# Kernel tuning notes

Hardware: AMD Instinct MI355X
Metric: run time of the kernel (lower is better)

Reference implementation:

```python
import math
import jax, jax.numpy as jnp
import numpy as np
from jax import lax

B, T, D, S, N_SLOTS, N_ITERS = 16, 4096, 768, 768, 16, 8
THR, EPS = 0.5, 1e-8
SCALE = D ** -0.5
NEG = -jnp.finfo(jnp.float32).max


def ln(x, g, b):
    mu = x.mean(-1, keepdims=True)
    var = ((x - mu) ** 2).mean(-1, keepdims=True)
    return (x - mu) / jnp.sqrt(var + 1e-5) * g + b


def gru_cell(u, h, wih, whh, bih, bhh):
    # torch GRUCell: r,z,n gate ordering
    gi = u @ wih.T + bih
    gh = h @ whh.T + bhh
    ir, iz, inn = jnp.split(gi, 3, axis=-1)
    hr, hz, hn = jnp.split(gh, 3, axis=-1)
    r = jax.nn.sigmoid(ir + hr)
    z = jax.nn.sigmoid(iz + hz)
    n = jnp.tanh(inn + r * hn)
    return (1.0 - z) * n + z * h


def sa_step(slots, k, v, p, slot_mask, context_mask):
    q = ln(slots, p['lsg'], p['lsb']) @ p['Wq'].T
    dots = jnp.einsum('bid,bjd->bij', q, k) * SCALE  # [B, n_slots, T]
    dots = jnp.where(context_mask[:, None, :], dots, NEG)
    if slot_mask is not None:
        dots = jnp.where(slot_mask[:, :, None], dots, NEG)
    attn_vis = jax.nn.softmax(dots, axis=1)  # softmax over SLOTS (inverted attn)
    attn = attn_vis + EPS
    attn = attn / attn.sum(-1, keepdims=True)
    updates = jnp.einsum('bjd,bij->bid', v, attn)
    b, n, d = slots.shape
    h = gru_cell(updates.reshape(b * n, d), slots.reshape(b * n, d),
                 p['gwih'], p['gwhh'], p['gbih'], p['gbhh'])
    slots = h.reshape(b, n, d)
    pre = ln(slots, p['lfg'], p['lfb'])
    slots = slots + (jax.nn.relu(pre @ p['w1'].T + p['b1']) @ p['w2'].T + p['b2'])
    return slots, attn_vis


def cluster_single(slots, attn, slot_mask):
    sl = lax.stop_gradient(slots)  # torch no_grad block
    ns = sl / jnp.clip(jnp.linalg.norm(sl, axis=-1, keepdims=True), 1e-12)
    smm = (slot_mask[:, :, None] & slot_mask[:, None, :]).astype(jnp.float32)
    dist = 1.0 - jnp.einsum('bnd,bmd->bnm', ns, ns)
    dist = jnp.where(smm > 0, dist, 2.0)
    adj = (dist < THR).astype(jnp.float32) * smm
    for _ in range(math.ceil(math.log2(N_SLOTS))):  # transitive closure by squaring
        adj = jnp.minimum(adj @ adj, 1.0) * smm
    cum = jnp.cumsum(adj, axis=1)
    cm = adj * (cum <= 1.0)  # keep first row of each connected component
    counts = (cm > 0).any(axis=2).sum(axis=1)
    reset = counts < 3
    eye = jnp.eye(N_SLOTS, dtype=jnp.float32)[None] * slot_mask[:, :, None].astype(jnp.float32)
    cm = jnp.where(reset[:, None, None], eye, cm)
    cw = cm / jnp.clip(cm.sum(axis=2, keepdims=True), 1.0)
    cm = lax.stop_gradient(cm)
    cw = lax.stop_gradient(cw)
    means = cw @ slots          # grads flow through slots only
    cattn = cm @ attn           # grads flow through attn only
    out_mask = (cm > 0).any(axis=2) & slot_mask
    return means, cattn, out_mask


def setup_inputs() -> dict:
    key = jax.random.key(0)
    ks = jax.random.split(key, 16)
    sc = 0.02
    return {
        'x': jax.random.normal(ks[0], (B, T, D), jnp.float32),
        'context_mask': jnp.ones((B, T), jnp.bool_),
        'n_slots': N_SLOTS,
        'slots_init': jax.random.normal(ks[1], (N_SLOTS, S), jnp.float32),
        'Wk': jax.random.normal(ks[2], (S, D), jnp.float32) * sc,
        'Wv': jax.random.normal(ks[3], (S, D), jnp.float32) * sc,
        'Wq': jax.random.normal(ks[4], (S, S), jnp.float32) * sc,
        'gwih': jax.random.normal(ks[5], (3 * S, S), jnp.float32) * sc,
        'gwhh': jax.random.normal(ks[6], (3 * S, S), jnp.float32) * sc,
        'gbih': jnp.zeros((3 * S,), jnp.float32),
        'gbhh': jnp.zeros((3 * S,), jnp.float32),
        'w1': jax.random.normal(ks[7], (4 * S, S), jnp.float32) * sc,
        'b1': jnp.zeros((4 * S,), jnp.float32),
        'w2': jax.random.normal(ks[8], (S, 4 * S), jnp.float32) * sc,
        'b2': jnp.zeros((S,), jnp.float32),
        'lin_g': jnp.ones((D,), jnp.float32), 'lin_b': jnp.zeros((D,), jnp.float32),
        'lsg': jnp.ones((S,), jnp.float32), 'lsb': jnp.zeros((S,), jnp.float32),
        'lfg': jnp.ones((S,), jnp.float32), 'lfb': jnp.zeros((S,), jnp.float32),
    }


def reference(x, context_mask, n_slots, slots_init, Wk, Wv, Wq, gwih, gwhh,
              gbih, gbhh, w1, b1, w2, b2, lin_g, lin_b, lsg, lsb, lfg, lfb):
    p = dict(Wq=Wq, gwih=gwih, gwhh=gwhh, gbih=gbih, gbhh=gbhh,
             w1=w1, b1=b1, w2=w2, b2=b2, lsg=lsg, lsb=lsb, lfg=lfg, lfb=lfb)
    xn = ln(x, lin_g, lin_b)
    init_slots = jnp.broadcast_to(slots_init[None], (x.shape[0], N_SLOTS, S))
    k = xn @ Wk.T
    v = xn @ Wv.T
    slots = init_slots
    for _ in range(N_ITERS):
        slots, attn = sa_step(slots, k, v, p, None, context_mask)
    # implicit differentiation trick
    slots = lax.stop_gradient(slots) - lax.stop_gradient(init_slots) + init_slots
    slot_mask = jnp.ones((x.shape[0], N_SLOTS), jnp.bool_)
    slots, attn = sa_step(slots, k, v, p, slot_mask, context_mask)
    slots, attn, slot_mask = cluster_single(slots, attn, slot_mask)
    attn_map = jnp.transpose(attn, (0, 2, 1))  # [B, T, n_slots]
    return slots, attn_map, slot_mask
```

## Files before the change

kernel.cpp:

```cpp
#include <hip/hip_runtime.h>
#include <hip/hip_bf16.h>

typedef __hip_bfloat16 bf16;
typedef __attribute__((ext_vector_type(4))) float f32x4;
typedef __attribute__((ext_vector_type(8))) short s16x8;
typedef unsigned int u32;
typedef unsigned short u16;

#define B_ 16
#define T_ 4096
#define D_ 768
#define S_ 768
#define NS 16
#define NIT 9
#define NCHUNK 16
#define TCH 256
#define EPS 1e-8f
#define SCALE 0.036084391824351615f

__device__ __forceinline__ void gld16(const void* g, void* l) {
    __builtin_amdgcn_global_load_lds((const __attribute__((address_space(1))) u32*)g,
                                     (__attribute__((address_space(3))) u32*)l, 16, 0, 0);
}

__device__ __forceinline__ u16 bfbits(float x) {
    bf16 h = __float2bfloat16(x);
    return *reinterpret_cast<u16*>(&h);
}

__global__ void __launch_bounds__(256) cvt_all_kernel(
    const float* __restrict__ wq, const float* __restrict__ wk, const float* __restrict__ wv,
    const float* __restrict__ gwih, const float* __restrict__ gwhh,
    const float* __restrict__ w1, const float* __restrict__ w2,
    bf16* __restrict__ wq_b, bf16* __restrict__ wkv_b,
    bf16* __restrict__ gwih_b, bf16* __restrict__ gwhh_b,
    bf16* __restrict__ w1_b, bf16* __restrict__ w2_b)
{
    int i = blockIdx.x * 256 + threadIdx.x;
    const int NW = 589824, NG = 1769472, NM = 2359296;
    if (i < NW) { wq_b[i] = __float2bfloat16(wq[i]); return; }
    i -= NW;
    if (i < NW) { wkv_b[i] = __float2bfloat16(wk[i]); return; }
    i -= NW;
    if (i < NW) { wkv_b[NW + i] = __float2bfloat16(wv[i]); return; }
    i -= NW;
    if (i < NG) { gwih_b[i] = __float2bfloat16(gwih[i]); return; }
    i -= NG;
    if (i < NG) { gwhh_b[i] = __float2bfloat16(gwhh[i]); return; }
    i -= NG;
    if (i < NM) { w1_b[i] = __float2bfloat16(w1[i]); return; }
    i -= NM;
    w2_b[i] = __float2bfloat16(w2[i]);
}

__global__ void __launch_bounds__(256) ln768_kernel(
    const float* __restrict__ x, const float* __restrict__ g,
    const float* __restrict__ bta, bf16* __restrict__ out)
{
    int row = blockIdx.x;
    int tid = threadIdx.x;
    const float* xr = x + (size_t)row * 768;
    float v0 = xr[tid], v1 = xr[tid + 256], v2 = xr[tid + 512];
    float s = v0 + v1 + v2;
    int lane = tid & 63, wid = tid >> 6;
    #pragma unroll
    for (int off = 32; off; off >>= 1) s += __shfl_down(s, off);
    __shared__ float red[4];
    __shared__ float sh_mu, sh_rs;
    if (lane == 0) red[wid] = s;
    __syncthreads();
    if (tid == 0) sh_mu = (red[0] + red[1] + red[2] + red[3]) * (1.f / 768.f);
    __syncthreads();
    float mu = sh_mu;
    float d0 = v0 - mu, d1 = v1 - mu, d2 = v2 - mu;
    float q = d0 * d0 + d1 * d1 + d2 * d2;
    #pragma unroll
    for (int off = 32; off; off >>= 1) q += __shfl_down(q, off);
    if (lane == 0) red[wid] = q;
    __syncthreads();
    if (tid == 0) sh_rs = rsqrtf((red[0] + red[1] + red[2] + red[3]) * (1.f / 768.f) + 1e-5f);
    __syncthreads();
    float rs = sh_rs;
    bf16* orow = out + (size_t)row * 768;
    orow[tid]       = __float2bfloat16(d0 * rs * g[tid]       + bta[tid]);
    orow[tid + 256] = __float2bfloat16(d1 * rs * g[tid + 256] + bta[tid + 256]);
    orow[tid + 512] = __float2bfloat16(d2 * rs * g[tid + 512] + bta[tid + 512]);
}

__global__ void __launch_bounds__(512) gemm256_kernel(
    const bf16* __restrict__ A, const bf16* __restrict__ W,
    bf16* __restrict__ kout, bf16* __restrict__ vTout, float* __restrict__ vsum)
{
    __shared__ char smem[49152];
    __shared__ float vs_l[128];
    bf16* As = (bf16*)smem;
    bf16* Bs = (bf16*)(smem + 32768);
    int tid = threadIdx.x, lane = tid & 63, wid = tid >> 6;
    int bid = blockIdx.x;
    int xcd = bid & 7, idx = bid >> 3;
    int mt = xcd * 32 + idx / 12;
    int nt = idx % 12;
    int bm0 = mt * 256, bn0 = nt * 128;
    int wr = wid >> 1, wc = wid & 1;
    int g = lane >> 4, r15 = lane & 15;
    const f32x4 vzero = {0.f, 0.f, 0.f, 0.f};
    f32x4 acc[4][4];
    #pragma unroll
    for (int m = 0; m < 4; ++m)
        #pragma unroll
        for (int n = 0; n < 4; ++n) acc[m][n] = vzero;

    for (int kt = 0; kt < 768; kt += 64) {
        __syncthreads();
        #pragma unroll
        for (int i = 0; i < 4; ++i) {
            int s0 = i * 512 + wid * 64;
            int o = (s0 + lane) * 16;
            int r = o >> 7, cb = o & 127;
            int cbs = cb ^ ((r & 7) << 4);
            gld16(A + (size_t)(bm0 + r) * 768 + kt + (cbs >> 1), (char*)As + (size_t)s0 * 16);
        }
        #pragma unroll
        for (int i = 0; i < 2; ++i) {
            int s0 = i * 512 + wid * 64;
            int o = (s0 + lane) * 16;
            int r = o >> 7, cb = o & 127;
            int cbs = cb ^ ((r & 7) << 4);
            gld16(W + (size_t)(bn0 + r) * 768 + kt + (cbs >> 1), (char*)Bs + (size_t)s0 * 16);
        }
        asm volatile("s_waitcnt vmcnt(0)" ::: "memory");
        __syncthreads();
        #pragma unroll
        for (int kk2 = 0; kk2 < 2; ++kk2) {
            s16x8 af[4], bfr[4];
            #pragma unroll
            for (int m = 0; m < 4; ++m) {
                int r = wr * 64 + m * 16 + r15;
                int p = r * 128 + ((kk2 * 64 + g * 16) ^ ((r & 7) << 4));
                af[m] = *(const s16x8*)((const char*)As + p);
            }
            #pragma unroll
            for (int n = 0; n < 4; ++n) {
                int r = wc * 64 + n * 16 + r15;
                int p = r * 128 + ((kk2 * 64 + g * 16) ^ ((r & 7) << 4));
                bfr[n] = *(const s16x8*)((const char*)Bs + p);
            }
            #pragma unroll
            for (int m = 0; m < 4; ++m)
                #pragma unroll
                for (int n = 0; n < 4; ++n)
                    acc[m][n] = __builtin_amdgcn_mfma_f32_16x16x32_bf16(af[m], bfr[n], acc[m][n], 0, 0, 0);
        }
    }

    bool is_v = (bn0 >= 768);
    float* Ct = (float*)smem;
    int bq = bm0 >> 12;
    int tloc = bm0 & 4095;
    if (is_v && tid < 128) vs_l[tid] = 0.f;
    #pragma unroll
    for (int q = 0; q < 4; ++q) {
        __syncthreads();
        if (wr == q) {
            #pragma unroll
            for (int m = 0; m < 4; ++m)
                #pragma unroll
                for (int n = 0; n < 4; ++n)
                    #pragma unroll
                    for (int j = 0; j < 4; ++j)
                        Ct[(m * 16 + g * 4 + j) * 132 + wc * 64 + n * 16 + r15] = acc[m][n][j];
        }
        __syncthreads();
        if (!is_v) {
            int r = tid >> 3, cq = tid & 7;
            u16 tmp[16];
            #pragma unroll
            for (int i = 0; i < 16; ++i) tmp[i] = bfbits(Ct[r * 132 + cq * 16 + i]);
            s16x8 o0, o1;
            #pragma unroll
            for (int i = 0; i < 8; ++i) { o0[i] = (short)tmp[i]; o1[i] = (short)tmp[8 + i]; }
            bf16* dst = kout + (size_t)(bm0 + q * 64 + r) * 768 + bn0 + cq * 16;
            *(s16x8*)dst = o0;
            *(s16x8*)(dst + 8) = o1;
        } else {
            int d = tid >> 2, tq = tid & 3;
            float ssum = 0.f;
            u16 tmp[16];
            #pragma unroll
            for (int i = 0; i < 16; ++i) {
                float f = Ct[(tq * 16 + i) * 132 + d];
                ssum += f;
                tmp[i] = bfbits(f);
            }
            s16x8 o0, o1;
            #pragma unroll
            for (int i = 0; i < 8; ++i) { o0[i] = (short)tmp[i]; o1[i] = (short)tmp[8 + i]; }
            bf16* dst = vTout + ((size_t)bq * 768 + (bn0 - 768) + d) * (size_t)T_
                        + tloc + q * 64 + tq * 16;
            *(s16x8*)dst = o0;
            *(s16x8*)(dst + 8) = o1;
            atomicAdd(&vs_l[d], ssum);
        }
    }
    if (is_v) {
        __syncthreads();
        if (tid < 128) atomicAdd(vsum + bq * 768 + (bn0 - 768) + tid, vs_l[tid]);
    }
}

__global__ void init_slots_kernel(const float* __restrict__ si,
                                  float* __restrict__ slots, bf16* __restrict__ slots_bf)
{
    int idx = blockIdx.x * 256 + threadIdx.x;
    float v = si[idx % (NS * S_)];
    slots[idx] = v;
    slots_bf[idx] = __float2bfloat16(v);
}

__global__ void __launch_bounds__(256) ln_gemm_kernel(
    const float* __restrict__ xin, const float* __restrict__ gam, const float* __restrict__ bet,
    const bf16* __restrict__ W, const float* __restrict__ bias,
    bf16* __restrict__ out, int N, int relu)
{
    __shared__ bf16 As[16 * 768];
    __shared__ bf16 Ws[2][64 * 64];
    int tid = threadIdx.x;
    int bx = blockIdx.x, bn0 = blockIdx.y * 64;
    int row = tid >> 4, li = tid & 15;
    const float* xr = xin + (size_t)(bx * 16 + row) * 768;
    float vals[48];
    float s = 0.f;
    #pragma unroll
    for (int i = 0; i < 48; ++i) { vals[i] = xr[li + i * 16]; s += vals[i]; }
    #pragma unroll
    for (int m = 1; m < 16; m <<= 1) s += __shfl_xor(s, m);
    float mu = s * (1.f / 768.f);
    float q = 0.f;
    #pragma unroll
    for (int i = 0; i < 48; ++i) { float d = vals[i] - mu; q += d * d; }
    #pragma unroll
    for (int m = 1; m < 16; m <<= 1) q += __shfl_xor(q, m);
    float rs = rsqrtf(q * (1.f / 768.f) + 1e-5f);
    #pragma unroll
    for (int i = 0; i < 48; ++i) {
        int c = li + i * 16;
        float v = (vals[i] - mu) * rs * gam[c] + bet[c];
        *(u16*)((char*)As + row * 1536 + ((c * 2) ^ ((row & 7) << 4))) = bfbits(v);
    }
    int lane = tid & 63, wid = tid >> 6;
    int g = lane >> 4, s15 = lane & 15;
    auto stageW = [&](int kt, int buf) {
        #pragma unroll
        for (int i = 0; i < 2; ++i) {
            int s0 = i * 256 + wid * 64;
            int o = (s0 + lane) * 16;
            int r = o >> 7, cb = o & 127;
            int cbs = cb ^ ((r & 7) << 4);
            gld16(W + (size_t)(bn0 + r) * 768 + kt + (cbs >> 1),
                  (char*)Ws[buf] + (size_t)s0 * 16);
        }
    };
    stageW(0, 0);
    asm volatile("s_waitcnt vmcnt(0)" ::: "memory");
    __syncthreads();
    f32x4 acc = {0.f, 0.f, 0.f, 0.f};
    int rb = wid * 16 + s15;
    for (int t = 0; t < 12; ++t) {
        int cur = t & 1;
        if (t < 11) stageW((t + 1) * 64, cur ^ 1);
        #pragma unroll
        for (int kk2 = 0; kk2 < 2; ++kk2) {
            int kabs = t * 64 + kk2 * 32;
            s16x8 af = *(const s16x8*)((const char*)As + s15 * 1536 +
                                       ((kabs * 2 + g * 16) ^ ((s15 & 7) << 4)));
            s16x8 bf_ = *(const s16x8*)((const char*)Ws[cur] + rb * 128 +
                                        ((kk2 * 64 + g * 16) ^ ((rb & 7) << 4)));
            acc = __builtin_amdgcn_mfma_f32_16x16x32_bf16(af, bf_, acc, 0, 0, 0);
        }
        asm volatile("s_waitcnt vmcnt(0)" ::: "memory");
        __syncthreads();
    }
    int cn = bn0 + rb;
    float bv = bias ? bias[cn] : 0.f;
    #pragma unroll
    for (int j = 0; j < 4; ++j) {
        float val = acc[j] + bv;
        if (relu) val = fmaxf(val, 0.f);
        out[(size_t)(bx * 16 + g * 4 + j) * N + cn] = __float2bfloat16(val);
    }
}

__device__ __forceinline__ void skinny_body(
    const bf16* A, const bf16* Bm, const float* bias, const float* Cin,
    float* Cf, bf16* Cb, int N, int K, int bm0, int bn0, int relu,
    bf16* As, bf16* Bs)
{
    int tid = threadIdx.x, lane = tid & 63, wid = tid >> 6;
    int g = lane >> 4, r15 = lane & 15;
    f32x4 acc = {0.f, 0.f, 0.f, 0.f};
    for (int kt = 0; kt < K; kt += 64) {
        __syncthreads();
        #pragma unroll
        for (int i = 0; i < 3; ++i) {
            int s0 = i * 256 + wid * 64;
            if (s0 < 640) {
                int o = (s0 + lane) * 16;
                if (o < 2048) {
                    int r = o >> 7, cb = o & 127;
                    int cbs = cb ^ ((r & 7) << 4);
                    gld16(A + (size_t)(bm0 + r) * K + kt + (cbs >> 1), (char*)As + (size_t)s0 * 16);
                } else {
                    int ob = o - 2048;
                    int r = ob >> 7, cb = ob & 127;
                    int cbs = cb ^ ((r & 7) << 4);
                    gld16(Bm + (size_t)(bn0 + r) * K + kt + (cbs >> 1),
                          (char*)Bs + (size_t)(s0 * 16 - 2048));
                }
            }
        }
        asm volatile("s_waitcnt vmcnt(0)" ::: "memory");
        __syncthreads();
        #pragma unroll
        for (int kk = 0; kk < 64; kk += 32) {
            int pa = r15 * 128 + ((kk * 2 + g * 16) ^ ((r15 & 7) << 4));
            s16x8 af = *(const s16x8*)((const char*)As + pa);
            int rb = wid * 16 + r15;
            int pb = rb * 128 + ((kk * 2 + g * 16) ^ ((rb & 7) << 4));
            s16x8 bfr = *(const s16x8*)((const char*)Bs + pb);
            acc = __builtin_amdgcn_mfma_f32_16x16x32_bf16(af, bfr, acc, 0, 0, 0);
        }
    }
    int cn = bn0 + wid * 16 + r15;
    float bv = bias ? bias[cn] : 0.f;
    #pragma unroll
    for (int j = 0; j < 4; ++j) {
        int cm = bm0 + g * 4 + j;
        size_t ci = (size_t)cm * N + cn;
        float val = acc[j] + bv;
        if (Cin) val += Cin[ci];
        if (relu) val = fmaxf(val, 0.f);
        if (Cf) Cf[ci] = val;
        if (Cb) Cb[ci] = __float2bfloat16(val);
    }
}

__global__ void __launch_bounds__(256) mlp2_kernel(
    const bf16* __restrict__ h1, const bf16* __restrict__ W2, const float* __restrict__ b2,
    const float* __restrict__ slotsB, float* __restrict__ slotsA, bf16* __restrict__ slotsA_bf)
{
    __shared__ bf16 As[16 * 64];
    __shared__ bf16 Bs[64 * 64];
    skinny_body(h1, W2, b2, slotsB, slotsA, slotsA_bf, 768, 3072,
                blockIdx.x * 16, blockIdx.y * 64, 0, As, Bs);
}

__global__ void __launch_bounds__(256) gru_gemm_kernel(
    const bf16* __restrict__ upd, const bf16* __restrict__ slots_bf,
    const bf16* __restrict__ Wih, const bf16* __restrict__ Whh,
    const float* __restrict__ bih, const float* __restrict__ bhh,
    float* __restrict__ gi, float* __restrict__ gh)
{
    __shared__ bf16 As[16 * 64];
    __shared__ bf16 Bs[64 * 64];
    int y = blockIdx.y;
    if (y < 36)
        skinny_body(upd, Wih, bih, nullptr, gi, nullptr, 2304, 768,
                    blockIdx.x * 16, y * 64, 0, As, Bs);
    else
        skinny_body(slots_bf, Whh, bhh, nullptr, gh, nullptr, 2304, 768,
                    blockIdx.x * 16, (y - 36) * 64, 0, As, Bs);
}

__global__ void __launch_bounds__(256) fused_attn_kernel(
    const bf16* __restrict__ q_bf, const bf16* __restrict__ k_bf, const bf16* __restrict__ vT,
    float* __restrict__ pU, float* __restrict__ prs, float* __restrict__ avis, int write_avis)
{
    __shared__ char smem[131072];
    bf16* ks0 = (bf16*)smem;
    bf16* ks1 = (bf16*)(smem + 49152);
    bf16* qs  = (bf16*)(smem + 98304);
    char* aL  = smem + 122880;
    __shared__ float rsw[2][16];
    int tid = threadIdx.x, lane = tid & 63, wid = tid >> 6;
    int b = blockIdx.x >> 4, chunk = blockIdx.x & 15;
    int t0 = chunk * TCH;
    int g = lane >> 4, s15 = lane & 15;
    const bf16* qb  = q_bf + (size_t)b * 16 * 768;
    const bf16* kb  = k_bf + (size_t)b * T_ * 768;
    const bf16* vtb = vT + (size_t)b * 768 * T_;

    auto stage_k = [&](int tb, bf16* dst) {
        #pragma unroll
        for (int i = 0; i < 12; ++i) {
            int s0 = i * 256 + wid * 64;
            int o = (s0 + lane) * 16;
            int r = o / 1536, cb = o % 1536;
            int cbs = cb ^ ((r & 7) << 4);
            gld16(kb + (size_t)(tb + r) * 768 + (cbs >> 1), (char*)dst + (size_t)s0 * 16);
        }
    };
    auto stage_v = [&](int tb, bf16* dst) {
        #pragma unroll
        for (int i = 0; i < 12; ++i) {
            int s0 = i * 256 + wid * 64;
            int o = (s0 + lane) * 16;
            int d = o >> 6, cb = o & 63;
            int cbs = cb ^ ((d & 3) << 4);
            gld16(vtb + (size_t)d * T_ + tb + (cbs >> 1), (char*)dst + (size_t)s0 * 16);
        }
    };

    #pragma unroll
    for (int i = 0; i < 6; ++i) {
        int s0 = i * 256 + wid * 64;
        int o = (s0 + lane) * 16;
        int r = o / 1536, cb = o % 1536;
        int cbs = cb ^ ((r & 7) << 4);
        gld16(qb + (size_t)r * 768 + (cbs >> 1), (char*)qs + (size_t)s0 * 16);
    }
    stage_k(t0, ks0);
    asm volatile("s_waitcnt vmcnt(0)" ::: "memory");
    __syncthreads();

    const f32x4 vzero = {0.f, 0.f, 0.f, 0.f};
    float rs_acc = 0.f;

    for (int ts = 0; ts < 8; ++ts) {
        bf16* cur = (ts & 1) ? ks1 : ks0;
        bf16* nxt = (ts & 1) ? ks0 : ks1;
        if (ts < 7) stage_k(t0 + (ts + 1) * 32, nxt);
        if (wid < 2) {
            f32x4 dacc = vzero;
            #pragma unroll
            for (int kk = 0; kk < 768; kk += 32) {
                int rk = wid * 16 + s15;
                int pk = rk * 1536 + ((kk * 2 + g * 16) ^ ((rk & 7) << 4));
                s16x8 kf = *(const s16x8*)((const char*)cur + pk);
                int pq = s15 * 1536 + ((kk * 2 + g * 16) ^ ((s15 & 7) << 4));
                s16x8 qf = *(const s16x8*)((const char*)qs + pq);
                dacc = __builtin_amdgcn_mfma_f32_16x16x32_bf16(kf, qf, dacc, 0, 0, 0);
            }
            float d0 = dacc[0] * SCALE, d1 = dacc[1] * SCALE,
                  d2 = dacc[2] * SCALE, d3 = dacc[3] * SCALE;
            float m0 = d0, m1 = d1, m2 = d2, m3 = d3;
            #pragma unroll
            for (int off = 1; off < 16; off <<= 1) {
                m0 = fmaxf(m0, __shfl_xor(m0, off));
                m1 = fmaxf(m1, __shfl_xor(m1, off));
                m2 = fmaxf(m2, __shfl_xor(m2, off));
                m3 = fmaxf(m3, __shfl_xor(m3, off));
            }
            float e0 = expf(d0 - m0), e1 = expf(d1 - m1), e2 = expf(d2 - m2), e3 = expf(d3 - m3);
            float q0 = e0, q1 = e1, q2 = e2, q3 = e3;
            #pragma unroll
            for (int off = 1; off < 16; off <<= 1) {
                q0 += __shfl_xor(q0, off);
                q1 += __shfl_xor(q1, off);
                q2 += __shfl_xor(q2, off);
                q3 += __shfl_xor(q3, off);
            }
            float a0 = e0 / q0, a1 = e1 / q1, a2 = e2 / q2, a3 = e3 / q3;
            rs_acc += a0 + a1 + a2 + a3;
            int tl = wid * 16 + g * 4;
            ushort2 p0, p1;
            p0.x = bfbits(a0); p0.y = bfbits(a1);
            p1.x = bfbits(a2); p1.y = bfbits(a3);
            int sw = (s15 & 3) << 4;
            char* aS = aL + ts * 1024;
            *(ushort2*)(aS + s15 * 64 + ((tl * 2) ^ sw))       = p0;
            *(ushort2*)(aS + s15 * 64 + (((tl + 2) * 2) ^ sw)) = p1;
            if (write_avis) {
                f32x4 w = {a0, a1, a2, a3};
                *(f32x4*)(avis + (size_t)(b * 16 + s15) * T_ + t0 + ts * 32 + tl) = w;
            }
        }
        asm volatile("s_waitcnt vmcnt(0)" ::: "memory");
        __syncthreads();
    }

    f32x4 uacc[12];
    #pragma unroll
    for (int i = 0; i < 12; ++i) uacc[i] = vzero;
    stage_v(t0, ks0);
    asm volatile("s_waitcnt vmcnt(0)" ::: "memory");
    __syncthreads();
    for (int ts = 0; ts < 8; ++ts) {
        bf16* cur = (ts & 1) ? ks1 : ks0;
        bf16* nxt = (ts & 1) ? ks0 : ks1;
        if (ts < 7) stage_v(t0 + (ts + 1) * 32, nxt);
        {
            int pa = ts * 1024 + s15 * 64 + ((g * 16) ^ ((s15 & 3) << 4));
            s16x8 afr = *(const s16x8*)(aL + pa);
            #pragma unroll
            for (int i = 0; i < 12; ++i) {
                int d = (wid * 12 + i) * 16 + s15;
                int pv = d * 64 + ((g * 16) ^ ((d & 3) << 4));
                s16x8 vf = *(const s16x8*)((const char*)cur + pv);
                uacc[i] = __builtin_amdgcn_mfma_f32_16x16x32_bf16(vf, afr, uacc[i], 0, 0, 0);
            }
        }
        asm volatile("s_waitcnt vmcnt(0)" ::: "memory");
        __syncthreads();
    }

    float* pUb = pU + (size_t)(b * 16 + chunk) * 768 * 16;
    #pragma unroll
    for (int i = 0; i < 12; ++i) {
        int dbase = (wid * 12 + i) * 16 + g * 4;
        #pragma unroll
        for (int j = 0; j < 4; ++j)
            pUb[(size_t)(dbase + j) * 16 + s15] = uacc[i][j];
    }
    rs_acc += __shfl_xor(rs_acc, 16);
    rs_acc += __shfl_xor(rs_acc, 32);
    if (wid < 2 && lane < 16) rsw[wid][s15] = rs_acc;
    __syncthreads();
    if (tid < 16) prs[(b * 16 + chunk) * 16 + tid] = rsw[0][tid] + rsw[1][tid];
}

__global__ void __launch_bounds__(256) attn_reduce_kernel(
    const float* __restrict__ pU, const float* __restrict__ prs,
    const float* __restrict__ vsum, bf16* __restrict__ upd)
{
    int idx = blockIdx.x * 256 + threadIdx.x;
    int d = idx % 768;
    int s = (idx / 768) & 15;
    int b = idx / (768 * 16);
    float su = 0.f;
    #pragma unroll
    for (int c = 0; c < 16; ++c) su += pU[((size_t)(b * 16 + c) * 768 + d) * 16 + s];
    float rs = 0.f;
    #pragma unroll
    for (int c = 0; c < 16; ++c) rs += prs[(b * 16 + c) * 16 + s];
    float val = (su + EPS * vsum[b * 768 + d]) / (rs + T_ * EPS);
    upd[idx] = __float2bfloat16(val);
}

__global__ void __launch_bounds__(256) gru_gates_kernel(
    const float* __restrict__ gi, const float* __restrict__ gh,
    const float* __restrict__ slotsA, float* __restrict__ slotsB)
{
    int idx = blockIdx.x * 256 + threadIdx.x;
    int r = idx / 768, c = idx - r * 768;
    const float* gir = gi + (size_t)r * 2304;
    const float* ghr = gh + (size_t)r * 2304;
    float ir = gir[c], iz = gir[768 + c], inn = gir[1536 + c];
    float hr = ghr[c], hz = ghr[768 + c], hn  = ghr[1536 + c];
    float rg = 1.f / (1.f + expf(-(ir + hr)));
    float z  = 1.f / (1.f + expf(-(iz + hz)));
    float n  = tanhf(inn + rg * hn);
    float h  = slotsA[idx];
    slotsB[idx] = (1.f - z) * n + z * h;
}

__global__ void __launch_bounds__(256) cluster_kernel(
    const float* __restrict__ slots, float* __restrict__ out_slots,
    float* __restrict__ out_mask, float* __restrict__ cm_g)
{
    int b = blockIdx.x;
    __shared__ float s[16][768];
    __shared__ float inv[16];
    __shared__ float adj[16][16], tmp[16][16], cw[16][16];
    __shared__ int reset_s;
    const float* sb = slots + (size_t)b * 16 * 768;
    for (int i = threadIdx.x; i < 16 * 768; i += 256) s[i / 768][i % 768] = sb[i];
    __syncthreads();
    if (threadIdx.x < 16) {
        float q = 0.f;
        for (int d = 0; d < 768; ++d) q += s[threadIdx.x][d] * s[threadIdx.x][d];
        inv[threadIdx.x] = 1.f / fmaxf(sqrtf(q), 1e-12f);
    }
    __syncthreads();
    int n = threadIdx.x >> 4, m = threadIdx.x & 15;
    float dot = 0.f;
    for (int d = 0; d < 768; ++d) dot += s[n][d] * s[m][d];
    dot *= inv[n] * inv[m];
    adj[n][m] = ((1.f - dot) < 0.5f) ? 1.f : 0.f;
    __syncthreads();
    #pragma unroll
    for (int it = 0; it < 4; ++it) {
        float t = 0.f;
        #pragma unroll
        for (int j = 0; j < 16; ++j) t += adj[n][j] * adj[j][m];
        tmp[n][m] = fminf(t, 1.f);
        __syncthreads();
        adj[n][m] = tmp[n][m];
        __syncthreads();
    }
    if (threadIdx.x < 16) {
        int mm = threadIdx.x;
        float run = 0.f;
        for (int nn = 0; nn < 16; ++nn) {
            run += adj[nn][mm];
            tmp[nn][mm] = adj[nn][mm] * ((run <= 1.f) ? 1.f : 0.f);
        }
    }
    __syncthreads();
    if (threadIdx.x == 0) {
        int cnt = 0;
        for (int nn = 0; nn < 16; ++nn) {
            bool any = false;
            for (int j = 0; j < 16; ++j) any = any || (tmp[nn][j] > 0.f);
            cnt += any ? 1 : 0;
        }
        reset_s = (cnt < 3) ? 1 : 0;
    }
    __syncthreads();
    if (reset_s) tmp[n][m] = (n == m) ? 1.f : 0.f;
    __syncthreads();
    if (threadIdx.x < 16) {
        float rs = 0.f;
        for (int j = 0; j < 16; ++j) rs += tmp[threadIdx.x][j];
        rs = fmaxf(rs, 1.f);
        for (int j = 0; j < 16; ++j) cw[threadIdx.x][j] = tmp[threadIdx.x][j] / rs;
        bool any = false;
        for (int j = 0; j < 16; ++j) any = any || (tmp[threadIdx.x][j] > 0.f);
        out_mask[b * 16 + threadIdx.x] = any ? 1.f : 0.f;
    }
    cm_g[b * 256 + threadIdx.x] = tmp[n][m];
    __syncthreads();
    for (int i = threadIdx.x; i < 16 * 768; i += 256) {
        int nn = i / 768, d = i - nn * 768;
        float acc = 0.f;
        #pragma unroll
        for (int j = 0; j < 16; ++j) acc += cw[nn][j] * s[j][d];
        out_slots[(size_t)b * 16 * 768 + i] = acc;
    }
}

__global__ void __launch_bounds__(256) cattn_kernel(
    const float* __restrict__ av, const float* __restrict__ cm_g, float* __restrict__ out_attn)
{
    int b = blockIdx.y;
    int t = blockIdx.x * 256 + threadIdx.x;
    __shared__ float cm[16][16];
    cm[threadIdx.x >> 4][threadIdx.x & 15] = cm_g[b * 256 + threadIdx.x];
    __syncthreads();
    float avv[16];
    #pragma unroll
    for (int j = 0; j < 16; ++j) avv[j] = av[((size_t)b * 16 + j) * T_ + t];
    #pragma unroll
    for (int i = 0; i < 16; ++i) {
        float acc = 0.f;
        #pragma unroll
        for (int j = 0; j < 16; ++j) acc += cm[i][j] * avv[j];
        out_attn[((size_t)b * T_ + t) * 16 + i] = acc;
    }
}

extern "C" void kernel_launch(void* const* d_in, const int* in_sizes, int n_in,
                              void* d_out, int out_size, void* d_ws, size_t ws_size,
                              hipStream_t stream)
{
    const float* x    = (const float*)d_in[0];
    const float* si   = (const float*)d_in[3];
    const float* Wk   = (const float*)d_in[4];
    const float* Wv   = (const float*)d_in[5];
    const float* Wq   = (const float*)d_in[6];
    const float* gwih = (const float*)d_in[7];
    const float* gwhh = (const float*)d_in[8];
    const float* gbih = (const float*)d_in[9];
    const float* gbhh = (const float*)d_in[10];
    const float* w1   = (const float*)d_in[11];
    const float* b1   = (const float*)d_in[12];
    const float* w2   = (const float*)d_in[13];
    const float* b2   = (const float*)d_in[14];
    const float* ling = (const float*)d_in[15];
    const float* linb = (const float*)d_in[16];
    const float* lsg  = (const float*)d_in[17];
    const float* lsb  = (const float*)d_in[18];
    const float* lfg  = (const float*)d_in[19];
    const float* lfb  = (const float*)d_in[20];

    char* w = (char*)d_ws;
    size_t off = 0;
    auto alloc = [&](size_t bytes) { void* p = w + off; off += (bytes + 255) & ~(size_t)255; return p; };
    bf16* xn     = (bf16*)alloc((size_t)B_ * T_ * D_ * 2);
    bf16* k_bf   = (bf16*)alloc((size_t)B_ * T_ * S_ * 2);
    bf16* vT     = (bf16*)alloc((size_t)B_ * S_ * T_ * 2);
    float* avis  = (float*)alloc((size_t)B_ * NS * T_ * 4);
    float* pU    = (float*)alloc((size_t)B_ * NCHUNK * S_ * NS * 4);
    float* prs   = (float*)alloc((size_t)B_ * NCHUNK * NS * 4);
    float* vsum  = (float*)alloc((size_t)B_ * S_ * 4);
    float* slotsA = (float*)alloc((size_t)B_ * NS * S_ * 4);
    bf16* slotsA_bf = (bf16*)alloc((size_t)B_ * NS * S_ * 2);
    float* slotsB = (float*)alloc((size_t)B_ * NS * S_ * 4);
    bf16* q_bf   = (bf16*)alloc((size_t)B_ * NS * S_ * 2);
    bf16* upd_bf = (bf16*)alloc((size_t)B_ * NS * S_ * 2);
    float* gi    = (float*)alloc((size_t)B_ * NS * 3 * S_ * 4);
    float* gh    = (float*)alloc((size_t)B_ * NS * 3 * S_ * 4);
    bf16* h1_bf  = (bf16*)alloc((size_t)B_ * NS * 4 * S_ * 2);
    bf16* wq_bf  = (bf16*)alloc((size_t)S_ * S_ * 2);
    bf16* wkv_bf = (bf16*)alloc((size_t)1536 * D_ * 2);
    bf16* gwih_bf = (bf16*)alloc((size_t)3 * S_ * S_ * 2);
    bf16* gwhh_bf = (bf16*)alloc((size_t)3 * S_ * S_ * 2);
    bf16* w1_bf  = (bf16*)alloc((size_t)4 * S_ * S_ * 2);
    bf16* w2_bf  = (bf16*)alloc((size_t)S_ * 4 * S_ * 2);
    float* cm_g  = (float*)alloc((size_t)B_ * 256 * 4);

    float* out_slots = (float*)d_out;
    float* out_attn  = out_slots + (size_t)B_ * NS * S_;
    float* out_mask  = out_attn + (size_t)B_ * T_ * NS;

    cvt_all_kernel<<<39168, 256, 0, stream>>>(Wq, Wk, Wv, gwih, gwhh, w1, w2,
                                              wq_bf, wkv_bf, gwih_bf, gwhh_bf, w1_bf, w2_bf);

    ln768_kernel<<<B_ * T_, 256, 0, stream>>>(x, ling, linb, xn);

    (void)hipMemsetAsync(vsum, 0, (size_t)B_ * S_ * 4, stream);
    gemm256_kernel<<<3072, 512, 0, stream>>>(xn, wkv_bf, k_bf, vT, vsum);

    init_slots_kernel<<<(B_ * NS * S_) / 256, 256, 0, stream>>>(si, slotsA, slotsA_bf);

    for (int it = 0; it < NIT; ++it) {
        {
            dim3 g(16, 12);
            ln_gemm_kernel<<<g, 256, 0, stream>>>(slotsA, lsg, lsb, wq_bf, nullptr,
                                                  q_bf, 768, 0);
        }
        fused_attn_kernel<<<B_ * NCHUNK, 256, 0, stream>>>(q_bf, k_bf, vT, pU, prs, avis,
                                                           (it == NIT - 1) ? 1 : 0);
        attn_reduce_kernel<<<(B_ * NS * S_) / 256, 256, 0, stream>>>(pU, prs, vsum, upd_bf);
        {
            dim3 g(16, 72);
            gru_gemm_kernel<<<g, 256, 0, stream>>>(upd_bf, slotsA_bf, gwih_bf, gwhh_bf,
                                                   gbih, gbhh, gi, gh);
        }
        gru_gates_kernel<<<(B_ * NS * S_) / 256, 256, 0, stream>>>(gi, gh, slotsA, slotsB);
        {
            dim3 g(16, 48);
            ln_gemm_kernel<<<g, 256, 0, stream>>>(slotsB, lfg, lfb, w1_bf, b1,
                                                  h1_bf, 3072, 1);
        }
        {
            dim3 g(16, 12);
            mlp2_kernel<<<g, 256, 0, stream>>>(h1_bf, w2_bf, b2, slotsB, slotsA, slotsA_bf);
        }
    }

    cluster_kernel<<<B_, 256, 0, stream>>>(slotsA, out_slots, out_mask, cm_g);
    {
        dim3 g(T_ / 256, B_);
        cattn_kernel<<<g, 256, 0, stream>>>(avis, cm_g, out_attn);
    }
}
```

Measured before the change: 1.464 ms.

## Fuse GRU input/hidden GEMMs with gate math; vectorize input layernorm

Replaces the separate GRU GEMM kernel (which wrote fp32 gi/gh to global) and the gates kernel with a single kernel. Each block computes all six gate tiles for a 16x64 output patch and applies the GRU nonlinearity in registers, removing the intermediate buffers and one launch per iteration. The grid shrinks from 16x72 to 16x12 blocks with more work per block, which lowers parallelism. The input layernorm now processes one row per wave using float4 loads and wave shuffles, with no block barriers, and the k-tile epilogue reads LDS as vectors.

```diff
diff --git a/kernel.cpp b/kernel.cpp
--- a/kernel.cpp
+++ b/kernel.cpp
@@ -57,34 +57,41 @@
     const float* __restrict__ x, const float* __restrict__ g,
     const float* __restrict__ bta, bf16* __restrict__ out)
 {
-    int row = blockIdx.x;
-    int tid = threadIdx.x;
-    const float* xr = x + (size_t)row * 768;
-    float v0 = xr[tid], v1 = xr[tid + 256], v2 = xr[tid + 512];
-    float s = v0 + v1 + v2;
-    int lane = tid & 63, wid = tid >> 6;
-    #pragma unroll
-    for (int off = 32; off; off >>= 1) s += __shfl_down(s, off);
-    __shared__ float red[4];
-    __shared__ float sh_mu, sh_rs;
-    if (lane == 0) red[wid] = s;
-    __syncthreads();
-    if (tid == 0) sh_mu = (red[0] + red[1] + red[2] + red[3]) * (1.f / 768.f);
-    __syncthreads();
-    float mu = sh_mu;
-    float d0 = v0 - mu, d1 = v1 - mu, d2 = v2 - mu;
-    float q = d0 * d0 + d1 * d1 + d2 * d2;
-    #pragma unroll
-    for (int off = 32; off; off >>= 1) q += __shfl_down(q, off);
-    if (lane == 0) red[wid] = q;
-    __syncthreads();
-    if (tid == 0) sh_rs = rsqrtf((red[0] + red[1] + red[2] + red[3]) * (1.f / 768.f) + 1e-5f);
-    __syncthreads();
-    float rs = sh_rs;
-    bf16* orow = out + (size_t)row * 768;
-    orow[tid]       = __float2bfloat16(d0 * rs * g[tid]       + bta[tid]);
-    orow[tid + 256] = __float2bfloat16(d1 * rs * g[tid + 256] + bta[tid + 256]);
-    orow[tid + 512] = __float2bfloat16(d2 * rs * g[tid + 512] + bta[tid + 512]);
+    int wid = threadIdx.x >> 6, lane = threadIdx.x & 63;
+    int row = blockIdx.x * 4 + wid;
+    const float4* xr = (const float4*)(x + (size_t)row * 768);
+    float4 v[3];
+    float s = 0.f;
+    #pragma unroll
+    for (int i = 0; i < 3; ++i) {
+        v[i] = xr[lane + i * 64];
+        s += v[i].x + v[i].y + v[i].z + v[i].w;
+    }
+    #pragma unroll
+    for (int off = 1; off < 64; off <<= 1) s += __shfl_xor(s, off);
+    float mu = s * (1.f / 768.f);
+    float q = 0.f;
+    #pragma unroll
+    for (int i = 0; i < 3; ++i) {
+        float a = v[i].x - mu, b = v[i].y - mu, c = v[i].z - mu, d = v[i].w - mu;
+        q += a * a + b * b + c * c + d * d;
+    }
+    #pragma unroll
+    for (int off = 1; off < 64; off <<= 1) q += __shfl_xor(q, off);
+    float rs = rsqrtf(q * (1.f / 768.f) + 1e-5f);
+    ushort4* orow = (ushort4*)(out + (size_t)row * 768);
+    const float4* gg = (const float4*)g;
+    const float4* bb = (const float4*)bta;
+    #pragma unroll
+    for (int i = 0; i < 3; ++i) {
+        float4 gv = gg[lane + i * 64], bv = bb[lane + i * 64];
+        ushort4 o;
+        o.x = bfbits((v[i].x - mu) * rs * gv.x + bv.x);
+        o.y = bfbits((v[i].y - mu) * rs * gv.y + bv.y);
+        o.z = bfbits((v[i].z - mu) * rs * gv.z + bv.z);
+        o.w = bfbits((v[i].w - mu) * rs * gv.w + bv.w);
+        orow[lane + i * 64] = o;
+    }
 }
 
 __global__ void __launch_bounds__(512) gemm256_kernel(
@@ -175,7 +182,11 @@
             int r = tid >> 3, cq = tid & 7;
             u16 tmp[16];
             #pragma unroll
-            for (int i = 0; i < 16; ++i) tmp[i] = bfbits(Ct[r * 132 + cq * 16 + i]);
+            for (int i = 0; i < 4; ++i) {
+                f32x4 vv = *(const f32x4*)&Ct[r * 132 + cq * 16 + i * 4];
+                #pragma unroll
+                for (int jj = 0; jj < 4; ++jj) tmp[i * 4 + jj] = bfbits(vv[jj]);
+            }
             s16x8 o0, o1;
             #pragma unroll
             for (int i = 0; i < 8; ++i) { o0[i] = (short)tmp[i]; o1[i] = (short)tmp[8 + i]; }
@@ -287,6 +298,78 @@
         float val = acc[j] + bv;
         if (relu) val = fmaxf(val, 0.f);
         out[(size_t)(bx * 16 + g * 4 + j) * N + cn] = __float2bfloat16(val);
+    }
+}
+
+__global__ void __launch_bounds__(256) gru_fused16_kernel(
+    const bf16* __restrict__ upd, const bf16* __restrict__ slotsA_bf,
+    const bf16* __restrict__ Wih, const bf16* __restrict__ Whh,
+    const float* __restrict__ bih, const float* __restrict__ bhh,
+    const float* __restrict__ slotsA, float* __restrict__ slotsB)
+{
+    __shared__ char sm[53248];
+    int tid = threadIdx.x, lane = tid & 63, wid = tid >> 6;
+    int g = lane >> 4, r15 = lane & 15;
+    int bm0 = blockIdx.x * 16, bn0 = blockIdx.y * 64;
+    const f32x4 vz = {0.f, 0.f, 0.f, 0.f};
+    f32x4 acc[6] = {vz, vz, vz, vz, vz, vz};
+
+    for (int kt = 0; kt < 768; kt += 64) {
+        __syncthreads();
+        #pragma unroll
+        for (int i = 0; i < 13; ++i) {
+            int s0 = i * 256 + wid * 64;
+            int seg = s0 + lane;
+            const bf16* src;
+            if (seg < 256) {
+                int ls = seg & 127;
+                int o = ls * 16;
+                int r = o >> 7, cb = o & 127;
+                int cbs = cb ^ ((r & 7) << 4);
+                const bf16* base = (seg < 128) ? upd : slotsA_bf;
+                src = base + (size_t)(bm0 + r) * 768 + kt + (cbs >> 1);
+            } else {
+                int ws = seg - 256;
+                int p = ws >> 9, qq = ws & 511;
+                int o = qq * 16;
+                int r = o >> 7, cb = o & 127;
+                int cbs = cb ^ ((r & 7) << 4);
+                src = (p < 3)
+                    ? Wih + (size_t)(p * 768 + bn0 + r) * 768 + kt + (cbs >> 1)
+                    : Whh + (size_t)((p - 3) * 768 + bn0 + r) * 768 + kt + (cbs >> 1);
+            }
+            gld16(src, sm + (size_t)s0 * 16);
+        }
+        asm volatile("s_waitcnt vmcnt(0)" ::: "memory");
+        __syncthreads();
+        #pragma unroll
+        for (int kk2 = 0; kk2 < 2; ++kk2) {
+            int pa = r15 * 128 + ((kk2 * 64 + g * 16) ^ ((r15 & 7) << 4));
+            s16x8 au = *(const s16x8*)(sm + pa);
+            s16x8 ah = *(const s16x8*)(sm + 2048 + pa);
+            int rb = wid * 16 + r15;
+            int pb = rb * 128 + ((kk2 * 64 + g * 16) ^ ((rb & 7) << 4));
+            #pragma unroll
+            for (int p = 0; p < 6; ++p) {
+                s16x8 wf = *(const s16x8*)(sm + 4096 + p * 8192 + pb);
+                acc[p] = __builtin_amdgcn_mfma_f32_16x16x32_bf16(
+                    (p < 3) ? au : ah, wf, acc[p], 0, 0, 0);
+            }
+        }
+    }
+    int cn = bn0 + wid * 16 + r15;
+    float bir = bih[cn], biz = bih[768 + cn], bin_ = bih[1536 + cn];
+    float bhr = bhh[cn], bhz = bhh[768 + cn], bhn = bhh[1536 + cn];
+    #pragma unroll
+    for (int j = 0; j < 4; ++j) {
+        int m = bm0 + g * 4 + j;
+        float ir = acc[0][j] + bir, iz = acc[1][j] + biz, inn = acc[2][j] + bin_;
+        float hr = acc[3][j] + bhr, hz = acc[4][j] + bhz, hn = acc[5][j] + bhn;
+        float rg = 1.f / (1.f + expf(-(ir + hr)));
+        float z  = 1.f / (1.f + expf(-(iz + hz)));
+        float nn = tanhf(inn + rg * hn);
+        float h  = slotsA[(size_t)m * 768 + cn];
+        slotsB[(size_t)m * 768 + cn] = (1.f - z) * nn + z * h;
     }
 }
 
@@ -354,23 +437,6 @@
                 blockIdx.x * 16, blockIdx.y * 64, 0, As, Bs);
 }
 
-__global__ void __launch_bounds__(256) gru_gemm_kernel(
-    const bf16* __restrict__ upd, const bf16* __restrict__ slots_bf,
-    const bf16* __restrict__ Wih, const bf16* __restrict__ Whh,
-    const float* __restrict__ bih, const float* __restrict__ bhh,
-    float* __restrict__ gi, float* __restrict__ gh)
-{
-    __shared__ bf16 As[16 * 64];
-    __shared__ bf16 Bs[64 * 64];
-    int y = blockIdx.y;
-    if (y < 36)
-        skinny_body(upd, Wih, bih, nullptr, gi, nullptr, 2304, 768,
-                    blockIdx.x * 16, y * 64, 0, As, Bs);
-    else
-        skinny_body(slots_bf, Whh, bhh, nullptr, gh, nullptr, 2304, 768,
-                    blockIdx.x * 16, (y - 36) * 64, 0, As, Bs);
-}
-
 __global__ void __launch_bounds__(256) fused_attn_kernel(
     const bf16* __restrict__ q_bf, const bf16* __restrict__ k_bf, const bf16* __restrict__ vT,
     float* __restrict__ pU, float* __restrict__ prs, float* __restrict__ avis, int write_avis)
@@ -387,7 +453,7 @@
     int g = lane >> 4, s15 = lane & 15;
     const bf16* qb  = q_bf + (size_t)b * 16 * 768;
     const bf16* kb  = k_bf + (size_t)b * T_ * 768;
-    const bf16* vtb = vT + (size_t)b * 768 * T_;
+    const bf16* vtb = vT + (size_t)b * 768 * (size_t)T_;
 
     auto stage_k = [&](int tb, bf16* dst) {
         #pragma unroll
@@ -470,8 +536,8 @@
             *(ushort2*)(aS + s15 * 64 + ((tl * 2) ^ sw))       = p0;
             *(ushort2*)(aS + s15 * 64 + (((tl + 2) * 2) ^ sw)) = p1;
             if (write_avis) {
-                f32x4 w = {a0, a1, a2, a3};
-                *(f32x4*)(avis + (size_t)(b * 16 + s15) * T_ + t0 + ts * 32 + tl) = w;
+                f32x4 wv = {a0, a1, a2, a3};
+                *(f32x4*)(avis + (size_t)(b * 16 + s15) * T_ + t0 + ts * 32 + tl) = wv;
             }
         }
         asm volatile("s_waitcnt vmcnt(0)" ::: "memory");
@@ -536,23 +602,6 @@
     upd[idx] = __float2bfloat16(val);
 }
 
-__global__ void __launch_bounds__(256) gru_gates_kernel(
-    const float* __restrict__ gi, const float* __restrict__ gh,
-    const float* __restrict__ slotsA, float* __restrict__ slotsB)
-{
-    int idx = blockIdx.x * 256 + threadIdx.x;
-    int r = idx / 768, c = idx - r * 768;
-    const float* gir = gi + (size_t)r * 2304;
-    const float* ghr = gh + (size_t)r * 2304;
-    float ir = gir[c], iz = gir[768 + c], inn = gir[1536 + c];
-    float hr = ghr[c], hz = ghr[768 + c], hn  = ghr[1536 + c];
-    float rg = 1.f / (1.f + expf(-(ir + hr)));
-    float z  = 1.f / (1.f + expf(-(iz + hz)));
-    float n  = tanhf(inn + rg * hn);
-    float h  = slotsA[idx];
-    slotsB[idx] = (1.f - z) * n + z * h;
-}
-
 __global__ void __launch_bounds__(256) cluster_kernel(
     const float* __restrict__ slots, float* __restrict__ out_slots,
     float* __restrict__ out_mask, float* __restrict__ cm_g)
@@ -597,13 +646,13 @@
     }
     __syncthreads();
     if (threadIdx.x == 0) {
-        int cnt = 0;
+        int cnt2 = 0;
         for (int nn = 0; nn < 16; ++nn) {
             bool any = false;
             for (int j = 0; j < 16; ++j) any = any || (tmp[nn][j] > 0.f);
-            cnt += any ? 1 : 0;
-        }
-        reset_s = (cnt < 3) ? 1 : 0;
+            cnt2 += any ? 1 : 0;
+        }
+        reset_s = (cnt2 < 3) ? 1 : 0;
     }
     __syncthreads();
     if (reset_s) tmp[n][m] = (n == m) ? 1.f : 0.f;
@@ -687,8 +736,6 @@
     float* slotsB = (float*)alloc((size_t)B_ * NS * S_ * 4);
     bf16* q_bf   = (bf16*)alloc((size_t)B_ * NS * S_ * 2);
     bf16* upd_bf = (bf16*)alloc((size_t)B_ * NS * S_ * 2);
-    float* gi    = (float*)alloc((size_t)B_ * NS * 3 * S_ * 4);
-    float* gh    = (float*)alloc((size_t)B_ * NS * 3 * S_ * 4);
     bf16* h1_bf  = (bf16*)alloc((size_t)B_ * NS * 4 * S_ * 2);
     bf16* wq_bf  = (bf16*)alloc((size_t)S_ * S_ * 2);
     bf16* wkv_bf = (bf16*)alloc((size_t)1536 * D_ * 2);
@@ -705,7 +752,7 @@
     cvt_all_kernel<<<39168, 256, 0, stream>>>(Wq, Wk, Wv, gwih, gwhh, w1, w2,
                                               wq_bf, wkv_bf, gwih_bf, gwhh_bf, w1_bf, w2_bf);
 
-    ln768_kernel<<<B_ * T_, 256, 0, stream>>>(x, ling, linb, xn);
+    ln768_kernel<<<B_ * T_ / 4, 256, 0, stream>>>(x, ling, linb, xn);
 
     (void)hipMemsetAsync(vsum, 0, (size_t)B_ * S_ * 4, stream);
     gemm256_kernel<<<3072, 512, 0, stream>>>(xn, wkv_bf, k_bf, vT, vsum);
@@ -722,11 +769,10 @@
                                                            (it == NIT - 1) ? 1 : 0);
         attn_reduce_kernel<<<(B_ * NS * S_) / 256, 256, 0, stream>>>(pU, prs, vsum, upd_bf);
         {
-            dim3 g(16, 72);
-            gru_gemm_kernel<<<g, 256, 0, stream>>>(upd_bf, slotsA_bf, gwih_bf, gwhh_bf,
-                                                   gbih, gbhh, gi, gh);
-        }
-        gru_gates_kernel<<<(B_ * NS * S_) / 256, 256, 0, stream>>>(gi, gh, slotsA, slotsB);
+            dim3 g(16, 12);
+            gru_fused16_kernel<<<g, 256, 0, stream>>>(upd_bf, slotsA_bf, gwih_bf, gwhh_bf,
+                                                      gbih, gbhh, slotsA, slotsB);
+        }
         {
             dim3 g(16, 48);
             ln_gemm_kernel<<<g, 256, 0, stream>>>(slotsB, lfg, lfb, w1_bf, b1,
```

New measurement: 1.478 ms. No clear change (+1.0%).
